# Optimization experiments

Hardware: AMD Instinct MI355X
Metric: run time of the kernel (lower is better)

The kernel has to match this reference:

```python
import jax, jax.numpy as jnp
import numpy as np

IOU_THRESHOLD = 0.5  # default iou_threshold of nms/class_spec_nms


def _nms_keep_mask(boxes, scores, iou_threshold):
    """Faithful port of the hand-rolled greedy NMS.

    The torch version builds a variable-length index list; here we return the
    equivalent fixed-shape boolean keep mask over the N boxes (jit-friendly).
    """
    n = scores.shape[0]
    x1, y1, x2, y2 = boxes[:, 0], boxes[:, 1], boxes[:, 2], boxes[:, 3]
    areas = (x2 - x1) * (y2 - y1)                       # [N]
    # pairwise intersection via broadcasted min/max (same math as the matmul-
    # with-ones trick in the source, without materializing the ones matrices)
    xi = jnp.minimum(x2[:, None], x2[None, :]) - jnp.maximum(x1[:, None], x1[None, :])
    yi = jnp.minimum(y2[:, None], y2[None, :]) - jnp.maximum(y1[:, None], y1[None, :])
    inter = jnp.maximum(xi, 0.0) * jnp.maximum(yi, 0.0)  # [N,N]
    iou = inter / (areas[:, None] + areas[None, :] - inter)

    first_max = scores.max()
    first_min = scores.min()
    curr_idx0 = jnp.argmax(scores)

    # carry: (candidate mask, working scores copy, keep mask, curr max, curr idx)
    init = (scores < first_max, scores, jnp.zeros((n,), dtype=bool), first_max, curr_idx0)

    def cond(state):
        mask, _, _, cmax, _ = state
        return jnp.any(mask) & (cmax >= first_min)

    def body(state):
        mask, sc, keep, cmax, cidx = state
        mask = mask & (iou[cidx] <= iou_threshold)   # suppress overlaps with current max
        mask = mask.at[cidx].set(False)
        keep = keep.at[cidx].set(True)               # keep current max
        sc = jnp.where(mask, sc, first_min - 1.0)    # kill suppressed scores
        cidx = jnp.argmax(sc)
        return mask, sc, keep, sc[cidx], cidx

    _, _, keep, _, _ = jax.lax.while_loop(cond, body, init)
    return keep


def setup_inputs() -> dict:
    key = jax.random.key(0)
    k1, k2, k3, k4, k5, k6 = jax.random.split(key, 6)
    N = 4096    # pre-NMS candidate boxes
    L = 16384   # p3 locations for a 1024x1024 image at stride 8 (128*128)
    xy = jax.random.uniform(k1, (N, 2), dtype=jnp.float32) * 900.0
    wh = jax.random.uniform(k2, (N, 2), dtype=jnp.float32) * 100.0 + 1.0
    boxes = jnp.concatenate([xy, xy + wh], axis=1)          # valid x1<x2, y1<y2
    scores = jax.random.uniform(k3, (N,), dtype=jnp.float32)
    class_ids = jax.random.randint(k4, (N,), 0, 80, dtype=jnp.int32)
    locations = jax.random.uniform(k5, (L, 2), dtype=jnp.float32) * 1024.0
    deltas = jax.random.uniform(k6, (L, 4), dtype=jnp.float32)  # positive gt deltas
    return {"boxes": boxes, "scores": scores, "class_ids": class_ids,
            "locations": locations, "deltas": deltas, "stride": 8}


def reference(boxes, scores, class_ids, locations, deltas, stride):
    # ---- class_spec_nms: class-offset trick then plain NMS ----
    max_coordinate = boxes.max()
    offsets = class_ids.astype(boxes.dtype) * (max_coordinate + 1.0)
    boxes_for_nms = boxes + offsets[:, None]
    keep_mask = _nms_keep_mask(boxes_for_nms, scores, IOU_THRESHOLD)

    # ---- fcos_apply_deltas_to_locations ----
    clipped = jnp.maximum(deltas, 0.0)
    s = jnp.asarray(stride, dtype=deltas.dtype)
    px, py = locations[:, 0], locations[:, 1]
    pred_boxes = jnp.stack([px - clipped[:, 0] * s,
                            py - clipped[:, 1] * s,
                            px + clipped[:, 2] * s,
                            py + clipped[:, 3] * s], axis=1)  # [L,4]

    # ---- fcos_make_centerness_targets ----
    lr_min = jnp.minimum(deltas[:, 0], deltas[:, 2])
    tb_min = jnp.minimum(deltas[:, 1], deltas[:, 3])
    lr_max = jnp.maximum(deltas[:, 0], deltas[:, 2])
    tb_max = jnp.maximum(deltas[:, 1], deltas[:, 3])
    centerness = jnp.sqrt((lr_min * tb_min) / (lr_max * tb_max))
    centerness = jnp.where(jnp.all(deltas == -1.0, axis=1), -1.0, centerness)

    pred_out = jnp.concatenate([pred_boxes, centerness[:, None]], axis=1)  # [L,5]
    return keep_mask, pred_out
```

## Files before the change

### kernel.cpp

```cpp
#include <hip/hip_runtime.h>
#include <stdint.h>

#define NB 4096
#define NBLK 64
#define IOU_THR 0.5f
#define ECAP 1024
#define RANKB 256
#define NTRI (NBLK * (NBLK + 1) / 2)

typedef unsigned long long u64;

__device__ __forceinline__ u64 readlane64(u64 v, int lane) {
    unsigned lo = (unsigned)__builtin_amdgcn_readlane((int)(unsigned)(v & 0xffffffffull), lane);
    unsigned hi = (unsigned)__builtin_amdgcn_readlane((int)(unsigned)(v >> 32), lane);
    return ((u64)hi << 32) | (u64)lo;
}

__global__ void __launch_bounds__(256) fused_front(
        const float* __restrict__ boxes, const float* __restrict__ scores,
        const float* __restrict__ loc, const float* __restrict__ deltas,
        const int* __restrict__ stride_p,
        float* __restrict__ pred_out, float* __restrict__ maxc,
        int* __restrict__ sidx, int* __restrict__ counts) {
    __shared__ __align__(16) float sh[NB];
    __shared__ float red[4];
    int blk = blockIdx.x;
    int t = threadIdx.x;

    if (blk < 64) {
        int i = blk * 256 + t;
        float s = (float)stride_p[0];
        float2 p = ((const float2*)loc)[i];
        float4 d = ((const float4*)deltas)[i];
        float c0 = fmaxf(d.x, 0.f), c1 = fmaxf(d.y, 0.f);
        float c2 = fmaxf(d.z, 0.f), c3 = fmaxf(d.w, 0.f);
        float b0 = p.x - c0 * s;
        float b1 = p.y - c1 * s;
        float b2 = p.x + c2 * s;
        float b3 = p.y + c3 * s;
        float lr_min = fminf(d.x, d.z), tb_min = fminf(d.y, d.w);
        float lr_max = fmaxf(d.x, d.z), tb_max = fmaxf(d.y, d.w);
        float cent = sqrtf((lr_min * tb_min) / (lr_max * tb_max));
        if (d.x == -1.f && d.y == -1.f && d.z == -1.f && d.w == -1.f) cent = -1.f;
        float* o = pred_out + (size_t)i * 5;
        o[0] = b0; o[1] = b1; o[2] = b2; o[3] = b3; o[4] = cent;
    } else if (blk < 64 + RANKB) {
        for (int i = t; i < NB; i += 256) sh[i] = scores[i];
        __syncthreads();
        int wave = t >> 6, lane = t & 63;
        int base = (blk - 64) * 16 + wave * 4;
        float my0 = sh[base + 0], my1 = sh[base + 1];
        float my2 = sh[base + 2], my3 = sh[base + 3];
        int c0 = 0, c1 = 0, c2 = 0, c3 = 0;
#pragma unroll 8
        for (int k = 0; k < 64; ++k) {
            int j = lane + k * 64;
            float sj = sh[j];
            c0 += (sj > my0) || (sj == my0 && j < base + 0);
            c1 += (sj > my1) || (sj == my1 && j < base + 1);
            c2 += (sj > my2) || (sj == my2 && j < base + 2);
            c3 += (sj > my3) || (sj == my3 && j < base + 3);
        }
        for (int o = 32; o > 0; o >>= 1) {
            c0 += __shfl_down(c0, o); c1 += __shfl_down(c1, o);
            c2 += __shfl_down(c2, o); c3 += __shfl_down(c3, o);
        }
        if (lane == 0) {
            sidx[c0] = base + 0; sidx[c1] = base + 1;
            sidx[c2] = base + 2; sidx[c3] = base + 3;
        }
    } else {
        if (t < NBLK + 1) counts[t] = 0;
        float m = -3.0e38f;
        for (int i = t; i < NB * 4; i += 256) m = fmaxf(m, boxes[i]);
        for (int o = 32; o > 0; o >>= 1) m = fmaxf(m, __shfl_down(m, o));
        if ((t & 63) == 0) red[t >> 6] = m;
        __syncthreads();
        if (t == 0) *maxc = fmaxf(fmaxf(red[0], red[1]), fmaxf(red[2], red[3]));
    }
}

__global__ void __launch_bounds__(64) edge_kernel(
        const float* __restrict__ boxes, const int* __restrict__ cls,
        const float* __restrict__ maxc, const int* __restrict__ sidx,
        int* __restrict__ counts, uint4* __restrict__ entries,
        float* __restrict__ keep_out) {
    int idx = blockIdx.x, r = 0;
    while (idx >= NBLK - r) { idx -= NBLK - r; ++r; }
    int c = r + idx;

    __shared__ float4 cb[64];
    __shared__ float ca[64];
    __shared__ int islast;
    int t = threadIdx.x;
    float mc1 = maxc[0] + 1.0f;

    int jr = sidx[r * 64 + t];
    float offr = (float)cls[jr] * mc1;
    float4 rb = ((const float4*)boxes)[jr];
    rb.x += offr; rb.y += offr; rb.z += offr; rb.w += offr;
    float ra = (rb.z - rb.x) * (rb.w - rb.y);

    if (c == r) {
        cb[t] = rb; ca[t] = ra;
    } else {
        int jc = sidx[c * 64 + t];
        float offc = (float)cls[jc] * mc1;
        float4 b = ((const float4*)boxes)[jc];
        b.x += offc; b.y += offc; b.z += offc; b.w += offc;
        cb[t] = b; ca[t] = (b.z - b.x) * (b.w - b.y);
    }
    __syncthreads();

    u64 w = 0;
#pragma unroll 8
    for (int j = 0; j < 64; ++j) {
        float4 b = cb[j];
        float xi = fminf(rb.z, b.z) - fmaxf(rb.x, b.x);
        float yi = fminf(rb.w, b.w) - fmaxf(rb.y, b.y);
        float inter = fmaxf(xi, 0.f) * fmaxf(yi, 0.f);
        float iou = inter / (ra + ca[j] - inter);
        w |= (u64)(iou > IOU_THR) << j;
    }
    if (c == r) w &= ~(1ull << t);
    if (w) {
        int slot = atomicAdd(&counts[r], 1);
        if (slot < ECAP) {
            u64* e = (u64*)&entries[r * ECAP + slot];
            atomicExch(e,     (u64)(unsigned)(t | (c << 8)));
            atomicExch(e + 1, w);
        }
    }

    asm volatile("s_waitcnt vmcnt(0)" ::: "memory");
    if (t == 0) {
        int old = atomicAdd(&counts[NBLK], 1);
        islast = (old == NTRI - 1);
    }
    __syncthreads();
    if (!islast) return;
    __threadfence();

    const int lane = t;
    int cnt_l = counts[lane];
    u64 accv = 0;
    u64 keptall = 0;
    u64 self = 1ull << lane;

    uint4 cur = entries[lane];
    uint4 n1  = entries[ECAP + lane];
    for (int b = 0; b < NBLK; ++b) {
        uint4 n2;
        if (b < NBLK - 2) n2 = entries[(u64)(b + 2) * ECAP + lane];

        int cnt = __builtin_amdgcn_readlane(cnt_l, b);
        if (cnt > ECAP) cnt = ECAP;
        int cfast = cnt < 64 ? cnt : 64;

        u64 colw = self;
        for (int e = 0; e < cfast; ++e) {
            unsigned meta = (unsigned)__builtin_amdgcn_readlane((int)cur.x, e);
            int l = meta & 255, cw = meta >> 8;
            if (cw == b) {
                unsigned lo = (unsigned)__builtin_amdgcn_readlane((int)cur.z, e);
                unsigned hi = (unsigned)__builtin_amdgcn_readlane((int)cur.w, e);
                if (lane == l) colw |= ((u64)hi << 32) | lo;
            }
        }
        for (int e = 64; e < cnt; ++e) {
            uint4 x = entries[(u64)b * ECAP + e];
            int l = x.x & 255, cw = x.x >> 8;
            if (cw == b && lane == l) colw |= ((u64)x.w << 32) | x.z;
        }

        u64 rem = readlane64(accv, b);
        u64 avail = ~rem;
        u64 edges = colw & avail & ~self;
        u64 involved = __ballot(edges != 0ull) & avail;
        u64 keptm = avail & ~involved;
        u64 sub = involved;
        while (sub) {
            int i = (int)__builtin_ctzll(sub);
            keptm |= 1ull << i;
            u64 ci = readlane64(colw, i);
            sub &= ~(ci | (1ull << i));
        }
        if (lane == b) keptall = keptm;

        for (int e = 0; e < cfast; ++e) {
            unsigned meta = (unsigned)__builtin_amdgcn_readlane((int)cur.x, e);
            unsigned lo   = (unsigned)__builtin_amdgcn_readlane((int)cur.z, e);
            unsigned hi   = (unsigned)__builtin_amdgcn_readlane((int)cur.w, e);
            int l = meta & 255, cw = meta >> 8;
            if (((keptm >> l) & 1ull) && lane == cw) accv |= ((u64)hi << 32) | lo;
        }
        for (int e = 64; e < cnt; ++e) {
            uint4 x = entries[(u64)b * ECAP + e];
            int l = x.x & 255, cw = x.x >> 8;
            if (((keptm >> l) & 1ull) && lane == cw) accv |= ((u64)x.w << 32) | x.z;
        }
        cur = n1; n1 = n2;
    }

#pragma unroll 8
    for (int bb = 0; bb < NBLK; ++bb) {
        u64 kw = readlane64(keptall, bb);
        int oidx = sidx[bb * 64 + lane];
        keep_out[oidx] = ((kw >> lane) & 1ull) ? 1.0f : 0.0f;
    }
}

extern "C" void kernel_launch(void* const* d_in, const int* in_sizes, int n_in,
                              void* d_out, int out_size, void* d_ws, size_t ws_size,
                              hipStream_t stream) {
    const float* boxes   = (const float*)d_in[0];
    const float* scores  = (const float*)d_in[1];
    const int*   cls     = (const int*)d_in[2];
    const float* loc     = (const float*)d_in[3];
    const float* deltas  = (const float*)d_in[4];
    const int*   stride  = (const int*)d_in[5];

    float* out = (float*)d_out;
    float* keep_out = out;
    float* pred_out = out + NB;

    char* ws = (char*)d_ws;
    float* maxc    = (float*)ws;                     ws += 16;
    int*   sidx    = (int*)ws;                       ws += NB * sizeof(int);
    int*   counts  = (int*)ws;                       ws += (NBLK + 1) * sizeof(int) + 12;
    uint4* entries = (uint4*)ws;

    fused_front<<<64 + RANKB + 1, 256, 0, stream>>>(boxes, scores, loc, deltas, stride,
                                                    pred_out, maxc, sidx, counts);
    edge_kernel<<<NTRI, 64, 0, stream>>>(boxes, cls, maxc, sidx, counts, entries,
                                         keep_out);
}
```

Before: 125.4 us.

## Precompute sorted offset boxes and areas in rank blocks; hierarchical completion counter

After: 128.4 us. +2.4%, slower.

```diff
diff --git a/kernel.cpp b/kernel.cpp
--- a/kernel.cpp
+++ b/kernel.cpp
@@ -18,10 +18,12 @@
 
 __global__ void __launch_bounds__(256) fused_front(
         const float* __restrict__ boxes, const float* __restrict__ scores,
+        const int* __restrict__ cls,
         const float* __restrict__ loc, const float* __restrict__ deltas,
         const int* __restrict__ stride_p,
-        float* __restrict__ pred_out, float* __restrict__ maxc,
-        int* __restrict__ sidx, int* __restrict__ counts) {
+        float* __restrict__ pred_out, int* __restrict__ sidx,
+        float* __restrict__ sboxes, float* __restrict__ sareas,
+        int* __restrict__ counts ) {
     __shared__ __align__(16) float sh[NB];
     __shared__ float red[4];
     int blk = blockIdx.x;
@@ -46,7 +48,13 @@
         o[0] = b0; o[1] = b1; o[2] = b2; o[3] = b3; o[4] = cent;
     } else if (blk < 64 + RANKB) {
         for (int i = t; i < NB; i += 256) sh[i] = scores[i];
+        float m = -3.0e38f;
+        for (int i = t; i < NB * 4; i += 256) m = fmaxf(m, boxes[i]);
+        for (int o = 32; o > 0; o >>= 1) m = fmaxf(m, __shfl_down(m, o));
+        if ((t & 63) == 0) red[t >> 6] = m;
         __syncthreads();
+        float mc1 = fmaxf(fmaxf(red[0], red[1]), fmaxf(red[2], red[3])) + 1.0f;
+
         int wave = t >> 6, lane = t & 63;
         int base = (blk - 64) * 16 + wave * 4;
         float my0 = sh[base + 0], my1 = sh[base + 1];
@@ -66,25 +74,28 @@
             c2 += __shfl_down(c2, o); c3 += __shfl_down(c3, o);
         }
         if (lane == 0) {
-            sidx[c0] = base + 0; sidx[c1] = base + 1;
-            sidx[c2] = base + 2; sidx[c3] = base + 3;
+            int rk[4] = { c0, c1, c2, c3 };
+#pragma unroll
+            for (int k = 0; k < 4; ++k) {
+                int i = base + k, rank = rk[k];
+                sidx[rank] = i;
+                float off = (float)cls[i] * mc1;
+                float4 b = ((const float4*)boxes)[i];
+                b.x += off; b.y += off; b.z += off; b.w += off;
+                ((float4*)sboxes)[rank] = b;
+                sareas[rank] = (b.z - b.x) * (b.w - b.y);
+            }
         }
     } else {
-        if (t < NBLK + 1) counts[t] = 0;
-        float m = -3.0e38f;
-        for (int i = t; i < NB * 4; i += 256) m = fmaxf(m, boxes[i]);
-        for (int o = 32; o > 0; o >>= 1) m = fmaxf(m, __shfl_down(m, o));
-        if ((t & 63) == 0) red[t >> 6] = m;
-        __syncthreads();
-        if (t == 0) *maxc = fmaxf(fmaxf(red[0], red[1]), fmaxf(red[2], red[3]));
+        if (t < 2 * NBLK + 1) counts[t] = 0;
     }
 }
 
 __global__ void __launch_bounds__(64) edge_kernel(
-        const float* __restrict__ boxes, const int* __restrict__ cls,
-        const float* __restrict__ maxc, const int* __restrict__ sidx,
-        int* __restrict__ counts, uint4* __restrict__ entries,
-        float* __restrict__ keep_out) {
+        const float* __restrict__ sboxes, const float* __restrict__ sareas,
+        const int* __restrict__ sidx,
+        int* __restrict__ counts ,
+        uint4* __restrict__ entries, float* __restrict__ keep_out) {
     int idx = blockIdx.x, r = 0;
     while (idx >= NBLK - r) { idx -= NBLK - r; ++r; }
     int c = r + idx;
@@ -93,22 +104,14 @@
     __shared__ float ca[64];
     __shared__ int islast;
     int t = threadIdx.x;
-    float mc1 = maxc[0] + 1.0f;
-
-    int jr = sidx[r * 64 + t];
-    float offr = (float)cls[jr] * mc1;
-    float4 rb = ((const float4*)boxes)[jr];
-    rb.x += offr; rb.y += offr; rb.z += offr; rb.w += offr;
-    float ra = (rb.z - rb.x) * (rb.w - rb.y);
-
+
+    float4 rb = ((const float4*)sboxes)[r * 64 + t];
+    float ra = sareas[r * 64 + t];
     if (c == r) {
         cb[t] = rb; ca[t] = ra;
     } else {
-        int jc = sidx[c * 64 + t];
-        float offc = (float)cls[jc] * mc1;
-        float4 b = ((const float4*)boxes)[jc];
-        b.x += offc; b.y += offc; b.z += offc; b.w += offc;
-        cb[t] = b; ca[t] = (b.z - b.x) * (b.w - b.y);
+        cb[t] = ((const float4*)sboxes)[c * 64 + t];
+        ca[t] = sareas[c * 64 + t];
     }
     __syncthreads();
 
@@ -134,8 +137,12 @@
 
     asm volatile("s_waitcnt vmcnt(0)" ::: "memory");
     if (t == 0) {
-        int old = atomicAdd(&counts[NBLK], 1);
-        islast = (old == NTRI - 1);
+        islast = 0;
+        int old = atomicAdd(&counts[NBLK + r], 1);
+        if (old == (NBLK - r) - 1) {
+            int o2 = atomicAdd(&counts[2 * NBLK], 1);
+            islast = (o2 == NBLK - 1);
+        }
     }
     __syncthreads();
     if (!islast) return;
@@ -225,13 +232,15 @@
     float* pred_out = out + NB;
 
     char* ws = (char*)d_ws;
-    float* maxc    = (float*)ws;                     ws += 16;
     int*   sidx    = (int*)ws;                       ws += NB * sizeof(int);
-    int*   counts  = (int*)ws;                       ws += (NBLK + 1) * sizeof(int) + 12;
+    float* sboxes  = (float*)ws;                     ws += NB * 4 * sizeof(float);
+    float* sareas  = (float*)ws;                     ws += NB * sizeof(float);
+    int*   counts  = (int*)ws;                       ws += (2 * NBLK + 1) * sizeof(int) + 12;
     uint4* entries = (uint4*)ws;
 
-    fused_front<<<64 + RANKB + 1, 256, 0, stream>>>(boxes, scores, loc, deltas, stride,
-                                                    pred_out, maxc, sidx, counts);
-    edge_kernel<<<NTRI, 64, 0, stream>>>(boxes, cls, maxc, sidx, counts, entries,
+    fused_front<<<64 + RANKB + 1, 256, 0, stream>>>(boxes, scores, cls, loc, deltas,
+                                                    stride, pred_out, sidx, sboxes,
+                                                    sareas, counts);
+    edge_kernel<<<NTRI, 64, 0, stream>>>(sboxes, sareas, sidx, counts, entries,
                                          keep_out);
 }
```
